# Kernel optimization log

Measured on AMD Instinct MI355X. Metric: run time of the kernel, lower is better.

## Reference

```python
import jax, jax.numpy as jnp
import numpy as np

BN_EPS = 1e-5

def _batchnorm(h, gamma, beta):
    # PyTorch BatchNorm1d in training mode: biased batch statistics over dim 0
    mu = jnp.mean(h, axis=0)
    var = jnp.mean((h - mu) ** 2, axis=0)
    return (h - mu) * jax.lax.rsqrt(var + BN_EPS) * gamma + beta


def setup_inputs() -> dict:
    key = jax.random.key(0)
    ks = jax.random.split(key, 8)
    N, E, D = 50000, 800000, 128
    x = jax.random.normal(ks[0], (N, D), dtype=jnp.float32)
    edge_index = jax.random.randint(ks[1], (2, E), 0, N, dtype=jnp.int64)
    s1 = 1.0 / np.sqrt(D)
    W1 = jax.random.uniform(ks[2], (D, D), jnp.float32, -s1, s1)
    b1 = jax.random.uniform(ks[3], (D,), jnp.float32, -s1, s1)
    W2 = jax.random.uniform(ks[4], (D, D), jnp.float32, -s1, s1)
    b2 = jax.random.uniform(ks[5], (D,), jnp.float32, -s1, s1)
    g1 = jnp.ones((D,), jnp.float32); beta1 = jnp.zeros((D,), jnp.float32)
    g2 = jnp.ones((D,), jnp.float32); beta2 = jnp.zeros((D,), jnp.float32)
    eps = jnp.array([0.1], jnp.float32)
    return {"x": x, "edge_index": edge_index, "eps": eps,
            "W1": W1, "b1": b1, "g1": g1, "beta1": beta1,
            "W2": W2, "b2": b2, "g2": g2, "beta2": beta2}


def reference(x, edge_index, eps, W1, b1, g1, beta1, W2, b2, g2, beta2):
    src, dst = edge_index[0], edge_index[1]
    N = x.shape[0]
    # gather by src, scatter-add to dst
    aggr = jax.ops.segment_sum(x[src], dst, num_segments=N)
    out = (1.0 + eps) * x + aggr  # eps broadcast (shape [1])
    h = jax.nn.relu(_batchnorm(out @ W1 + b1, g1, beta1))
    h = jax.nn.relu(_batchnorm(h @ W2 + b2, g2, beta2))
    return h
```

## Files before the change

kernel.cpp:

```cpp
#include <hip/hip_runtime.h>

#define D 128
#define FB2 8192
#define GCAP 512
#define NBMAX 3328
#define SCAN_PER 13

typedef __attribute__((ext_vector_type(8))) short short8;
typedef __attribute__((ext_vector_type(4))) float f32x4;

static __device__ __forceinline__ unsigned short f2bf(float f) {
    union { float f; unsigned u; } v; v.f = f;
    unsigned r = v.u + 0x7FFF + ((v.u >> 16) & 1);
    return (unsigned short)(r >> 16);
}

static __device__ __forceinline__ float2 bfpair2f(unsigned p) {
    union { unsigned u; float f; } a, b;
    a.u = (p & 0xFFFFu) << 16;
    b.u = p & 0xFFFF0000u;
    return make_float2(a.f, b.f);
}

static __device__ __forceinline__ void acc2(f32x4& A, uint2 p) {
    union { unsigned u; float f; } t;
    float f0, f1, f2, f3;
    t.u = p.x << 16;          f0 = t.f;
    t.u = p.x & 0xFFFF0000u;  f1 = t.f;
    t.u = p.y << 16;          f2 = t.f;
    t.u = p.y & 0xFFFF0000u;  f3 = t.f;
    A[0] += f0; A[1] += f1; A[2] += f2; A[3] += f3;
}

static __device__ __forceinline__ void emit_row(
    unsigned* h0, int d, unsigned lane8, float epsv, uint2 xv, f32x4 A)
{
    union { unsigned u; float f; } t;
    float x0, x1, x2, x3;
    t.u = xv.x << 16;          x0 = t.f;
    t.u = xv.x & 0xFFFF0000u;  x1 = t.f;
    t.u = xv.y << 16;          x2 = t.f;
    t.u = xv.y & 0xFFFF0000u;  x3 = t.f;
    float r0 = fmaf(epsv, x0, A[0]);
    float r1 = fmaf(epsv, x1, A[1]);
    float r2 = fmaf(epsv, x2, A[2]);
    float r3 = fmaf(epsv, x3, A[3]);
    uint2 o;
    o.x = (unsigned)f2bf(r0) | ((unsigned)f2bf(r1) << 16);
    o.y = (unsigned)f2bf(r2) | ((unsigned)f2bf(r3) << 16);
    *(uint2*)((char*)h0 + ((unsigned)(d * 256) + lane8)) = o;
}

__global__ __launch_bounds__(256) void prep_kernel(
    const float4* __restrict__ x4, uint2* __restrict__ xh, int xtotal,
    const float* __restrict__ W1, const float* __restrict__ W2,
    unsigned short* __restrict__ Wf1, unsigned short* __restrict__ Wf2,
    float* __restrict__ stats, int* __restrict__ bucketCount,
    unsigned short* __restrict__ zrow, int xblocks)
{
    if (blockIdx.x < (unsigned)xblocks) {
        int i = blockIdx.x * 256 + threadIdx.x;
        if (i >= xtotal) return;
        float4 v = x4[i];
        uint2 o;
        o.x = (unsigned)f2bf(v.x) | ((unsigned)f2bf(v.y) << 16);
        o.y = (unsigned)f2bf(v.z) | ((unsigned)f2bf(v.w) << 16);
        xh[i] = o;
    } else if (blockIdx.x < (unsigned)(xblocks + 128)) {
        int idx = (blockIdx.x - xblocks) * 256 + threadIdx.x;
        const float* W = (idx < 16384) ? W1 : W2;
        unsigned short* Wf = (idx < 16384) ? Wf1 : Wf2;
        int e = idx & 16383;
        int j = e & 7, lane = (e >> 3) & 63, ckk = e >> 9;
        int ct = ckk & 7, kk = ckk >> 3;
        int k = kk * 32 + (lane >> 4) * 8 + j;
        int n = ct * 16 + (lane & 15);
        Wf[e] = f2bf(W[k * 128 + n]);
    } else {
        int t = threadIdx.x;
        stats[t] = 0.f; stats[t + 256] = 0.f;
        for (int i = t; i < NBMAX; i += 256) bucketCount[i] = 0;
        if (t < 128) zrow[t] = 0;
    }
}

__global__ __launch_bounds__(256) void bucket_hist_kernel(
    const int* __restrict__ ei, int E, int NB2, int* __restrict__ bucketCount)
{
    __shared__ int hist[NBMAX];
    int tid = threadIdx.x;
    for (int i = tid; i < NB2; i += 256) hist[i] = 0;
    __syncthreads();
    int b0 = blockIdx.x * FB2;
    int lim = min(FB2, E - b0);
    for (int i = tid; i < lim; i += 256)
        atomicAdd(&hist[ei[E + b0 + i] >> 4], 1);
    __syncthreads();
    for (int i = tid; i < NB2; i += 256)
        if (hist[i]) atomicAdd(&bucketCount[i], hist[i]);
}

__global__ __launch_bounds__(256) void bucket_scan_kernel(
    const int* __restrict__ bucketCount, int NB2, int E,
    int* __restrict__ bucketBase, int* __restrict__ bucketCursor)
{
    __shared__ int part[256];
    int tid = threadIdx.x;
    int loc[SCAN_PER];
    int s = 0;
    #pragma unroll
    for (int j = 0; j < SCAN_PER; ++j) {
        int idx = tid * SCAN_PER + j;
        int v = (idx < NB2) ? bucketCount[idx] : 0;
        loc[j] = s;
        s += v;
    }
    part[tid] = s;
    __syncthreads();
    #pragma unroll
    for (int off = 1; off < 256; off <<= 1) {
        int u = (tid >= off) ? part[tid - off] : 0;
        __syncthreads();
        part[tid] += u;
        __syncthreads();
    }
    int tb = (tid > 0) ? part[tid - 1] : 0;
    #pragma unroll
    for (int j = 0; j < SCAN_PER; ++j) {
        int idx = tid * SCAN_PER + j;
        if (idx < NB2) {
            int ex = tb + loc[j];
            bucketBase[idx] = ex;
            bucketCursor[idx] = ex;
        }
    }
    if (tid == 0) bucketBase[NB2] = E;
}

__global__ __launch_bounds__(256) void bucket_fill_kernel(
    const int* __restrict__ ei, int E, int NB2,
    int* __restrict__ bucketCursor, unsigned* __restrict__ rec)
{
    __shared__ int hist[NBMAX], base[NBMAX];
    int tid = threadIdx.x;
    int b0 = blockIdx.x * FB2;
    for (int i = tid; i < NB2; i += 256) hist[i] = 0;
    __syncthreads();
    int lim = min(FB2, E - b0);
    for (int i = tid; i < lim; i += 256)
        atomicAdd(&hist[ei[E + b0 + i] >> 4], 1);
    __syncthreads();
    for (int i = tid; i < NB2; i += 256) {
        int c = hist[i];
        base[i] = c ? atomicAdd(&bucketCursor[i], c) : 0;
        hist[i] = 0;
    }
    __syncthreads();
    for (int i = tid; i < lim; i += 256) {
        int e = b0 + i;
        int dst = ei[E + e], src = ei[e];
        int bk = dst >> 4;
        int r = atomicAdd(&hist[bk], 1);
        rec[base[bk] + r] = ((unsigned)src << 4) | (unsigned)(dst & 15);
    }
}

__global__ __launch_bounds__(256) void bucket_gather_kernel(
    const unsigned* __restrict__ xh, const unsigned* __restrict__ rec,
    const int* __restrict__ bucketBase, const float* __restrict__ epsp,
    unsigned* __restrict__ h0, int N, int zoff)
{
    int g = blockIdx.x;
    int tid = threadIdx.x;
    int d0 = g << 4;

    __shared__ int cnts[16], rnk[16], offs[17];
    __shared__ int slist[GCAP + 8];

    if (tid < 16) { cnts[tid] = 0; rnk[tid] = 0; }
    for (int i = tid; i < GCAP + 8; i += 256) slist[i] = zoff;
    __syncthreads();

    int lo = bucketBase[g], hi = bucketBase[g + 1];
    for (int i = lo + tid; i < hi; i += 256)
        atomicAdd(&cnts[rec[i] & 15], 1);
    __syncthreads();
    if (tid == 0) {
        int run = 0;
        #pragma unroll
        for (int i = 0; i < 16; ++i) {
            offs[i] = run;
            run += (cnts[i] + 7) & ~7;
            if (run > GCAP) run = GCAP;
        }
        offs[16] = run;
    }
    __syncthreads();
    for (int i = lo + tid; i < hi; i += 256) {
        unsigned r = rec[i];
        int d = r & 15;
        int rk = atomicAdd(&rnk[d], 1);
        int pos = offs[d] + rk;
        if (pos < offs[d + 1]) slist[pos] = (int)((r >> 4) << 8);
    }
    __syncthreads();

    int wv = tid >> 6, lane = tid & 63;
    int half = lane >> 5, l5 = lane & 31;
    unsigned lane8 = (unsigned)(l5 << 3);
    float epsv = 1.0f + __ldg(epsp);
    const char* xc = (const char*)xh;

    int dloc = wv * 4;
    int dA = d0 + dloc, dB = dA + 1, dC = dA + 2, dD = dA + 3;
    int vA = (dA < N), vB = (dB < N), vC = (dC < N), vD = (dD < N);

    int s0 = offs[dloc + 0], s1 = offs[dloc + 1];
    int s2 = offs[dloc + 2], s3 = offs[dloc + 3], s4 = offs[dloc + 4];
    int nch0 = (s1 - s0) >> 3, nch1 = (s2 - s1) >> 3;
    int nch2 = (s3 - s2) >> 3, nch3 = (s4 - s3) >> 3;
    int iters = max(max(nch0, nch1), max(nch2, nch3));

    uint2 xv0 = *(const uint2*)(xc + (unsigned)((vA ? dA : 0) * 256) + lane8);
    uint2 xv1 = *(const uint2*)(xc + (unsigned)((vB ? dB : 0) * 256) + lane8);
    uint2 xv2 = *(const uint2*)(xc + (unsigned)((vC ? dC : 0) * 256) + lane8);
    uint2 xv3 = *(const uint2*)(xc + (unsigned)((vD ? dD : 0) * 256) + lane8);

    f32x4 A0 = (f32x4){0.f, 0.f, 0.f, 0.f};
    f32x4 A1 = (f32x4){0.f, 0.f, 0.f, 0.f};
    f32x4 A2 = (f32x4){0.f, 0.f, 0.f, 0.f};
    f32x4 A3 = (f32x4){0.f, 0.f, 0.f, 0.f};

    for (int c = 0; c < iters; ++c) {
        int b0 = (c < nch0) ? (s0 + (c << 3)) : GCAP;
        int b1 = (c < nch1) ? (s1 + (c << 3)) : GCAP;
        int b2 = (c < nch2) ? (s2 + (c << 3)) : GCAP;
        int b3 = (c < nch3) ? (s3 + (c << 3)) : GCAP;
        uint2 p0[4], p1[4], p2[4], p3[4];
        #pragma unroll
        for (int k = 0; k < 4; ++k) {
            unsigned o0 = (unsigned)slist[b0 + 2 * k + half];
            unsigned o1 = (unsigned)slist[b1 + 2 * k + half];
            unsigned o2 = (unsigned)slist[b2 + 2 * k + half];
            unsigned o3 = (unsigned)slist[b3 + 2 * k + half];
            p0[k] = *(const uint2*)(xc + (o0 + lane8));
            p1[k] = *(const uint2*)(xc + (o1 + lane8));
            p2[k] = *(const uint2*)(xc + (o2 + lane8));
            p3[k] = *(const uint2*)(xc + (o3 + lane8));
        }
        #pragma unroll
        for (int k = 0; k < 4; ++k) {
            acc2(A0, p0[k]); acc2(A1, p1[k]);
            acc2(A2, p2[k]); acc2(A3, p3[k]);
        }
    }

    #pragma unroll
    for (int r = 0; r < 4; ++r) {
        A0[r] += __shfl_xor(A0[r], 32, 64);
        A1[r] += __shfl_xor(A1[r], 32, 64);
        A2[r] += __shfl_xor(A2[r], 32, 64);
        A3[r] += __shfl_xor(A3[r], 32, 64);
    }

    if (half == 0) {
        if (vA) emit_row(h0, dA, lane8, epsv, xv0, A0);
        if (vB) emit_row(h0, dB, lane8, epsv, xv1, A1);
        if (vC) emit_row(h0, dC, lane8, epsv, xv2, A2);
        if (vD) emit_row(h0, dD, lane8, epsv, xv3, A3);
    }
}

static __device__ __forceinline__ short8 bn_relu_pack(
    const unsigned short* arow, int c, const float* scf, const float* shf)
{
    uint4 rw = *(const uint4*)(arow + c);
    float2 p0 = bfpair2f(rw.x), p1 = bfpair2f(rw.y);
    float2 p2 = bfpair2f(rw.z), p3 = bfpair2f(rw.w);
    p0.x = fmaxf(fmaf(p0.x, scf[c + 0], shf[c + 0]), 0.f);
    p0.y = fmaxf(fmaf(p0.y, scf[c + 1], shf[c + 1]), 0.f);
    p1.x = fmaxf(fmaf(p1.x, scf[c + 2], shf[c + 2]), 0.f);
    p1.y = fmaxf(fmaf(p1.y, scf[c + 3], shf[c + 3]), 0.f);
    p2.x = fmaxf(fmaf(p2.x, scf[c + 4], shf[c + 4]), 0.f);
    p2.y = fmaxf(fmaf(p2.y, scf[c + 5], shf[c + 5]), 0.f);
    p3.x = fmaxf(fmaf(p3.x, scf[c + 6], shf[c + 6]), 0.f);
    p3.y = fmaxf(fmaf(p3.y, scf[c + 7], shf[c + 7]), 0.f);
    short8 af;
    af[0] = (short)f2bf(p0.x); af[1] = (short)f2bf(p0.y);
    af[2] = (short)f2bf(p1.x); af[3] = (short)f2bf(p1.y);
    af[4] = (short)f2bf(p2.x); af[5] = (short)f2bf(p2.y);
    af[6] = (short)f2bf(p3.x); af[7] = (short)f2bf(p3.y);
    return af;
}

__global__ __launch_bounds__(256) void gemm_bn_mfma_kernel(
    const unsigned short* __restrict__ a_bf,
    const float* __restrict__ stat_in, const float* __restrict__ gamma,
    const float* __restrict__ beta, float invN,
    const unsigned short* __restrict__ Wf, const float* __restrict__ bias,
    unsigned short* __restrict__ zout,
    float* __restrict__ stat_sum, float* __restrict__ stat_sq,
    int N, int mode)
{
    __shared__ unsigned short Wl[16384];
    __shared__ float part[1024];
    __shared__ float scf[128], shf[128];

    int tid = threadIdx.x;
    {
        float4* dst = (float4*)Wl;
        const float4* srcp = (const float4*)Wf;
        #pragma unroll
        for (int i = 0; i < 8; ++i) dst[tid + i * 256] = srcp[tid + i * 256];
    }
    if (mode == 1 && tid < 128) {
        float mean = stat_in[tid] * invN;
        float var  = stat_in[128 + tid] * invN - mean * mean;
        float sv = gamma[tid] * rsqrtf(var + 1e-5f);
        scf[tid] = sv;
        shf[tid] = fmaf(-mean, sv, beta[tid]);
    }
    __syncthreads();

    int w = tid >> 6, lane = tid & 63, q = lane >> 4, n16 = lane & 15;
    int rowb = blockIdx.x * 128 + w * 16;
    int m0 = rowb + n16;
    int m1 = rowb + 64 + n16;
    int mc0 = (m0 < N) ? m0 : (N - 1);
    int mc1 = (m1 < N) ? m1 : (N - 1);
    const unsigned short* arow0 = a_bf + (size_t)mc0 * D;
    const unsigned short* arow1 = a_bf + (size_t)mc1 * D;

    f32x4 acc0[8], acc1[8];
    #pragma unroll
    for (int ct = 0; ct < 8; ++ct) {
        acc0[ct] = (f32x4){0.f, 0.f, 0.f, 0.f};
        acc1[ct] = (f32x4){0.f, 0.f, 0.f, 0.f};
    }

    #pragma unroll
    for (int kk = 0; kk < 4; ++kk) {
        int c = kk * 32 + q * 8;
        short8 af0, af1;
        if (mode == 0) {
            af0 = *(const short8*)(arow0 + c);
            af1 = *(const short8*)(arow1 + c);
        } else {
            af0 = bn_relu_pack(arow0, c, scf, shf);
            af1 = bn_relu_pack(arow1, c, scf, shf);
        }
        #pragma unroll
        for (int ct = 0; ct < 8; ++ct) {
            short8 bf = *(const short8*)&Wl[(((kk * 8 + ct) * 64) + lane) * 8];
            acc0[ct] = __builtin_amdgcn_mfma_f32_16x16x32_bf16(af0, bf, acc0[ct], 0, 0, 0);
            acc1[ct] = __builtin_amdgcn_mfma_f32_16x16x32_bf16(af1, bf, acc1[ct], 0, 0, 0);
        }
    }

    #pragma unroll
    for (int ct = 0; ct < 8; ++ct) {
        int col = ct * 16 + n16;
        float bv = __ldg(bias + col);
        float s = 0.f, qs = 0.f;
        #pragma unroll
        for (int reg = 0; reg < 4; ++reg) {
            int row = rowb + q * 4 + reg;
            float v = acc0[ct][reg] + bv;
            if (row < N) {
                zout[(size_t)row * D + col] = f2bf(v);
                s += v;
                qs = fmaf(v, v, qs);
            }
        }
        #pragma unroll
        for (int reg = 0; reg < 4; ++reg) {
            int row = rowb + 64 + q * 4 + reg;
            float v = acc1[ct][reg] + bv;
            if (row < N) {
                zout[(size_t)row * D + col] = f2bf(v);
                s += v;
                qs = fmaf(v, v, qs);
            }
        }
        s  += __shfl_xor(s, 16, 64);
        s  += __shfl_xor(s, 32, 64);
        qs += __shfl_xor(qs, 16, 64);
        qs += __shfl_xor(qs, 32, 64);
        if (lane < 16) {
            part[w * 128 + col] = s;
            part[512 + w * 128 + col] = qs;
        }
    }
    __syncthreads();

    if (tid < 128) {
        float s  = part[tid] + part[128 + tid] + part[256 + tid] + part[384 + tid];
        float qq = part[512 + tid] + part[640 + tid] + part[768 + tid] + part[896 + tid];
        atomicAdd(&stat_sum[tid], s);
        atomicAdd(&stat_sq[tid], qq);
    }
}

__global__ __launch_bounds__(256) void bn_relu_kernel(
    const uint2* __restrict__ z2, float4* __restrict__ out,
    const float* __restrict__ stat2, const float* __restrict__ gamma,
    const float* __restrict__ beta, float invN, int total4)
{
    __shared__ float sf[128], tf[128];
    int tid = threadIdx.x;
    if (tid < 128) {
        float mean = stat2[tid] * invN;
        float var  = stat2[128 + tid] * invN - mean * mean;
        float sv = gamma[tid] * rsqrtf(var + 1e-5f);
        sf[tid] = sv;
        tf[tid] = fmaf(-mean, sv, beta[tid]);
    }
    __syncthreads();

    int i = blockIdx.x * 256 + tid;
    if (i >= total4) return;
    uint2 zp = z2[i];
    float2 v01 = bfpair2f(zp.x);
    float2 v23 = bfpair2f(zp.y);
    int c = (i & 31) * 4;
    float4 o;
    o.x = fmaxf(fmaf(v01.x, sf[c + 0], tf[c + 0]), 0.f);
    o.y = fmaxf(fmaf(v01.y, sf[c + 1], tf[c + 1]), 0.f);
    o.z = fmaxf(fmaf(v23.x, sf[c + 2], tf[c + 2]), 0.f);
    o.w = fmaxf(fmaf(v23.y, sf[c + 3], tf[c + 3]), 0.f);
    out[i] = o;
}

extern "C" void kernel_launch(void* const* d_in, const int* in_sizes, int n_in,
                              void* d_out, int out_size, void* d_ws, size_t ws_size,
                              hipStream_t stream)
{
    const float* x   = (const float*)d_in[0];
    const int*   ei  = (const int*)d_in[1];
    const float* eps = (const float*)d_in[2];
    const float* W1  = (const float*)d_in[3];
    const float* b1  = (const float*)d_in[4];
    const float* g1  = (const float*)d_in[5];
    const float* be1 = (const float*)d_in[6];
    const float* W2  = (const float*)d_in[7];
    const float* b2  = (const float*)d_in[8];
    const float* g2  = (const float*)d_in[9];
    const float* be2 = (const float*)d_in[10];

    int N = in_sizes[0] / D;
    int E = in_sizes[1] / 2;
    size_t ND = (size_t)N * D;
    int NB2 = (N + 15) >> 4;

    unsigned short* xh  = (unsigned short*)d_ws;
    unsigned short* z1  = xh;
    unsigned short* region2 = xh + ND + 128;
    unsigned* rec       = (unsigned*)region2;
    unsigned short* z2  = region2;
    int* bucketCount    = (int*)((char*)region2 + (4 << 20));
    int* bucketBase     = bucketCount + NBMAX;
    int* bucketCursor   = bucketBase + NBMAX + 1;
    float* stats        = (float*)(region2 + ND);
    unsigned short* Wf1 = (unsigned short*)(stats + 512);
    unsigned short* Wf2 = Wf1 + 16384;

    float* sum1 = stats + 0,   *sq1 = stats + 128;
    float* sum2 = stats + 256, *sq2 = stats + 384;
    unsigned short* h0 = (unsigned short*)d_out;

    int xtotal = N * 32;
    int xblocks = (xtotal + 255) / 256;
    prep_kernel<<<xblocks + 129, 256, 0, stream>>>(
        (const float4*)x, (uint2*)xh, xtotal, W1, W2, Wf1, Wf2,
        stats, bucketCount, xh + ND, xblocks);

    int fblocks = (E + FB2 - 1) / FB2;
    bucket_hist_kernel<<<fblocks, 256, 0, stream>>>(ei, E, NB2, bucketCount);
    bucket_scan_kernel<<<1, 256, 0, stream>>>(bucketCount, NB2, E, bucketBase, bucketCursor);
    bucket_fill_kernel<<<fblocks, 256, 0, stream>>>(ei, E, NB2, bucketCursor, rec);
    bucket_gather_kernel<<<NB2, 256, 0, stream>>>(
        (const unsigned*)xh, rec, bucketBase, eps, (unsigned*)h0, N, N * 256);

    int gblocks = (N + 127) / 128;
    gemm_bn_mfma_kernel<<<gblocks, 256, 0, stream>>>(
        h0, nullptr, nullptr, nullptr, 0.f,
        Wf1, b1, z1, sum1, sq1, N, 0);
    gemm_bn_mfma_kernel<<<gblocks, 256, 0, stream>>>(
        z1, sum1, g1, be1, 1.0f / N,
        Wf2, b2, z2, sum2, sq2, N, 1);
    bn_relu_kernel<<<(N * 32 + 255) / 256, 256, 0, stream>>>(
        (const uint2*)z2, (float4*)d_out, sum2, g2, be2, 1.0f / N, N * 32);
}
```

Measured before the change: 229.5 us.

## Switch to two-level bucket sort with coarse buckets and replicated BN stat accumulators

Edges are now bucketed into 128-destination coarse buckets (about 391 instead of about 3125), which shrinks the shared histograms and the scan. A new subsort pass then orders each bucket by destination and records per-destination offsets, so the gather kernel no longer recounts or ranks edges with shared atomics. BN statistic accumulation is also spread across 4 replicated slots chosen by block index to cut global atomic contention, and readers sum the replicas. The cost is an extra kernel launch plus an extra pass over the edge records through a second buffer. There is also an aliasing risk: rec2 sits at an 8 MB offset inside region2, so it may overlap the bucket arrays or z2 for large E.

```diff
diff --git a/kernel.cpp b/kernel.cpp
--- a/kernel.cpp
+++ b/kernel.cpp
@@ -3,8 +3,7 @@
 #define D 128
 #define FB2 8192
 #define GCAP 512
-#define NBMAX 3328
-#define SCAN_PER 13
+#define NREP 4
 
 typedef __attribute__((ext_vector_type(8))) short short8;
 typedef __attribute__((ext_vector_type(4))) float f32x4;
@@ -78,79 +77,67 @@
         Wf[e] = f2bf(W[k * 128 + n]);
     } else {
         int t = threadIdx.x;
-        stats[t] = 0.f; stats[t + 256] = 0.f;
-        for (int i = t; i < NBMAX; i += 256) bucketCount[i] = 0;
+        #pragma unroll
+        for (int i = 0; i < 2 * NREP; ++i) stats[t + i * 256] = 0.f;
+        bucketCount[t] = 0; bucketCount[t + 256] = 0;
         if (t < 128) zrow[t] = 0;
     }
 }
 
 __global__ __launch_bounds__(256) void bucket_hist_kernel(
-    const int* __restrict__ ei, int E, int NB2, int* __restrict__ bucketCount)
-{
-    __shared__ int hist[NBMAX];
+    const int* __restrict__ ei, int E, int NB, int* __restrict__ bucketCount)
+{
+    __shared__ int hist[512];
     int tid = threadIdx.x;
-    for (int i = tid; i < NB2; i += 256) hist[i] = 0;
+    for (int i = tid; i < NB; i += 256) hist[i] = 0;
     __syncthreads();
     int b0 = blockIdx.x * FB2;
     int lim = min(FB2, E - b0);
     for (int i = tid; i < lim; i += 256)
-        atomicAdd(&hist[ei[E + b0 + i] >> 4], 1);
-    __syncthreads();
-    for (int i = tid; i < NB2; i += 256)
+        atomicAdd(&hist[ei[E + b0 + i] >> 7], 1);
+    __syncthreads();
+    for (int i = tid; i < NB; i += 256)
         if (hist[i]) atomicAdd(&bucketCount[i], hist[i]);
 }
 
-__global__ __launch_bounds__(256) void bucket_scan_kernel(
-    const int* __restrict__ bucketCount, int NB2, int E,
+__global__ __launch_bounds__(512) void bucket_scan_kernel(
+    const int* __restrict__ bucketCount, int NB, int E,
     int* __restrict__ bucketBase, int* __restrict__ bucketCursor)
 {
-    __shared__ int part[256];
+    __shared__ int sm[512];
     int tid = threadIdx.x;
-    int loc[SCAN_PER];
-    int s = 0;
+    int v = (tid < NB) ? bucketCount[tid] : 0;
+    sm[tid] = v;
+    __syncthreads();
     #pragma unroll
-    for (int j = 0; j < SCAN_PER; ++j) {
-        int idx = tid * SCAN_PER + j;
-        int v = (idx < NB2) ? bucketCount[idx] : 0;
-        loc[j] = s;
-        s += v;
-    }
-    part[tid] = s;
-    __syncthreads();
-    #pragma unroll
-    for (int off = 1; off < 256; off <<= 1) {
-        int u = (tid >= off) ? part[tid - off] : 0;
+    for (int off = 1; off < 512; off <<= 1) {
+        int u = (tid >= off) ? sm[tid - off] : 0;
         __syncthreads();
-        part[tid] += u;
+        sm[tid] += u;
         __syncthreads();
     }
-    int tb = (tid > 0) ? part[tid - 1] : 0;
-    #pragma unroll
-    for (int j = 0; j < SCAN_PER; ++j) {
-        int idx = tid * SCAN_PER + j;
-        if (idx < NB2) {
-            int ex = tb + loc[j];
-            bucketBase[idx] = ex;
-            bucketCursor[idx] = ex;
-        }
-    }
-    if (tid == 0) bucketBase[NB2] = E;
+    if (tid < NB) {
+        int ex = sm[tid] - v;
+        bucketBase[tid] = ex;
+        bucketCursor[tid] = ex;
+    }
+    if (tid == 0) bucketBase[NB] = E;
 }
 
 __global__ __launch_bounds__(256) void bucket_fill_kernel(
-    const int* __restrict__ ei, int E, int NB2,
+    const int* __restrict__ ei, int E, int NB,
     int* __restrict__ bucketCursor, unsigned* __restrict__ rec)
 {
-    __shared__ int hist[NBMAX], base[NBMAX];
+    __shared__ int hist[512], base[512];
     int tid = threadIdx.x;
     int b0 = blockIdx.x * FB2;
-    for (int i = tid; i < NB2; i += 256) hist[i] = 0;
+    for (int i = tid; i < NB; i += 256) hist[i] = 0;
     __syncthreads();
     int lim = min(FB2, E - b0);
     for (int i = tid; i < lim; i += 256)
-        atomicAdd(&hist[ei[E + b0 + i] >> 4], 1);
-    __syncthreads();
-    for (int i = tid; i < NB2; i += 256) {
+        atomicAdd(&hist[ei[E + b0 + i] >> 7], 1);
+    __syncthreads();
+    for (int i = tid; i < NB; i += 256) {
         int c = hist[i];
         base[i] = c ? atomicAdd(&bucketCursor[i], c) : 0;
         hist[i] = 0;
@@ -159,49 +146,70 @@
     for (int i = tid; i < lim; i += 256) {
         int e = b0 + i;
         int dst = ei[E + e], src = ei[e];
-        int bk = dst >> 4;
+        int bk = dst >> 7;
         int r = atomicAdd(&hist[bk], 1);
-        rec[base[bk] + r] = ((unsigned)src << 4) | (unsigned)(dst & 15);
+        rec[base[bk] + r] = ((unsigned)src << 7) | (unsigned)(dst & 127);
+    }
+}
+
+__global__ __launch_bounds__(256) void subsort_kernel(
+    const unsigned* __restrict__ rec, const int* __restrict__ bucketBase,
+    unsigned* __restrict__ rec2, int* __restrict__ dstOff)
+{
+    __shared__ int cnt[128], pref[128], rnk[128];
+    int b = blockIdx.x, tid = threadIdx.x;
+    int lo = bucketBase[b], hi = bucketBase[b + 1];
+    if (tid < 128) { cnt[tid] = 0; rnk[tid] = 0; }
+    __syncthreads();
+    for (int i = lo + tid; i < hi; i += 256)
+        atomicAdd(&cnt[rec[i] & 127], 1);
+    __syncthreads();
+    if (tid == 0) {
+        int run = 0;
+        #pragma unroll
+        for (int j = 0; j < 128; ++j) { pref[j] = run; run += cnt[j]; }
+    }
+    __syncthreads();
+    if (tid < 128) dstOff[b * 128 + tid] = lo + pref[tid];
+    for (int i = lo + tid; i < hi; i += 256) {
+        unsigned r = rec[i];
+        int d = r & 127;
+        int rk = atomicAdd(&rnk[d], 1);
+        rec2[lo + pref[d] + rk] = ((r >> 7) << 8) | (unsigned)(d & 15);
     }
 }
 
 __global__ __launch_bounds__(256) void bucket_gather_kernel(
-    const unsigned* __restrict__ xh, const unsigned* __restrict__ rec,
-    const int* __restrict__ bucketBase, const float* __restrict__ epsp,
+    const unsigned* __restrict__ xh, const unsigned* __restrict__ rec2,
+    const int* __restrict__ dstOff, const float* __restrict__ epsp,
     unsigned* __restrict__ h0, int N, int zoff)
 {
     int g = blockIdx.x;
     int tid = threadIdx.x;
     int d0 = g << 4;
 
-    __shared__ int cnts[16], rnk[16], offs[17];
+    __shared__ int doff[17], offs[17];
     __shared__ int slist[GCAP + 8];
 
-    if (tid < 16) { cnts[tid] = 0; rnk[tid] = 0; }
+    if (tid < 17) doff[tid] = dstOff[d0 + tid];
     for (int i = tid; i < GCAP + 8; i += 256) slist[i] = zoff;
-    __syncthreads();
-
-    int lo = bucketBase[g], hi = bucketBase[g + 1];
-    for (int i = lo + tid; i < hi; i += 256)
-        atomicAdd(&cnts[rec[i] & 15], 1);
     __syncthreads();
     if (tid == 0) {
         int run = 0;
         #pragma unroll
-        for (int i = 0; i < 16; ++i) {
-            offs[i] = run;
-            run += (cnts[i] + 7) & ~7;
+        for (int j = 0; j < 16; ++j) {
+            offs[j] = run;
+            run += (doff[j + 1] - doff[j] + 7) & ~7;
             if (run > GCAP) run = GCAP;
         }
         offs[16] = run;
     }
     __syncthreads();
-    for (int i = lo + tid; i < hi; i += 256) {
-        unsigned r = rec[i];
-        int d = r & 15;
-        int rk = atomicAdd(&rnk[d], 1);
-        int pos = offs[d] + rk;
-        if (pos < offs[d + 1]) slist[pos] = (int)((r >> 4) << 8);
+    for (int i = doff[0] + tid; i < doff[16]; i += 256) {
+        unsigned r = rec2[i];
+        int dl = r & 15;
+        int slot = offs[dl] + (i - doff[dl]);
+        if (slot < offs[dl + 1]) slist[slot] = (int)(r & 0xFFFFFF00u);
     }
     __syncthreads();
 
@@ -314,8 +322,14 @@
         for (int i = 0; i < 8; ++i) dst[tid + i * 256] = srcp[tid + i * 256];
     }
     if (mode == 1 && tid < 128) {
-        float mean = stat_in[tid] * invN;
-        float var  = stat_in[128 + tid] * invN - mean * mean;
+        float ssum = 0.f, sqs = 0.f;
+        #pragma unroll
+        for (int r = 0; r < NREP; ++r) {
+            ssum += stat_in[r * 512 + tid];
+            sqs  += stat_in[r * 512 + 128 + tid];
+        }
+        float mean = ssum * invN;
+        float var  = sqs * invN - mean * mean;
         float sv = gamma[tid] * rsqrtf(var + 1e-5f);
         scf[tid] = sv;
         shf[tid] = fmaf(-mean, sv, beta[tid]);
@@ -394,10 +408,11 @@
     __syncthreads();
 
     if (tid < 128) {
+        int rep = ((int)blockIdx.x & (NREP - 1)) * 512;
         float s  = part[tid] + part[128 + tid] + part[256 + tid] + part[384 + tid];
         float qq = part[512 + tid] + part[640 + tid] + part[768 + tid] + part[896 + tid];
-        atomicAdd(&stat_sum[tid], s);
-        atomicAdd(&stat_sq[tid], qq);
+        atomicAdd(&stat_sum[rep + tid], s);
+        atomicAdd(&stat_sq[rep + tid], qq);
     }
 }
 
@@ -409,8 +424,14 @@
     __shared__ float sf[128], tf[128];
     int tid = threadIdx.x;
     if (tid < 128) {
-        float mean = stat2[tid] * invN;
-        float var  = stat2[128 + tid] * invN - mean * mean;
+        float ssum = 0.f, sqs = 0.f;
+        #pragma unroll
+        for (int r = 0; r < NREP; ++r) {
+            ssum += stat2[r * 512 + tid];
+            sqs  += stat2[r * 512 + 128 + tid];
+        }
+        float mean = ssum * invN;
+        float var  = sqs * invN - mean * mean;
         float sv = gamma[tid] * rsqrtf(var + 1e-5f);
         sf[tid] = sv;
         tf[tid] = fmaf(-mean, sv, beta[tid]);
@@ -450,7 +471,8 @@
     int N = in_sizes[0] / D;
     int E = in_sizes[1] / 2;
     size_t ND = (size_t)N * D;
-    int NB2 = (N + 15) >> 4;
+    int NB  = (N + 127) >> 7;
+    int NG  = (N + 15) >> 4;
 
     unsigned short* xh  = (unsigned short*)d_ws;
     unsigned short* z1  = xh;
@@ -458,10 +480,12 @@
     unsigned* rec       = (unsigned*)region2;
     unsigned short* z2  = region2;
     int* bucketCount    = (int*)((char*)region2 + (4 << 20));
-    int* bucketBase     = bucketCount + NBMAX;
-    int* bucketCursor   = bucketBase + NBMAX + 1;
+    int* bucketBase     = bucketCount + 512;
+    int* bucketCursor   = bucketBase + 513;
+    int* dstOff         = bucketCursor + 512;
+    unsigned* rec2      = (unsigned*)((char*)region2 + (8 << 20));
     float* stats        = (float*)(region2 + ND);
-    unsigned short* Wf1 = (unsigned short*)(stats + 512);
+    unsigned short* Wf1 = (unsigned short*)(stats + 2 * NREP * 256);
     unsigned short* Wf2 = Wf1 + 16384;
 
     float* sum1 = stats + 0,   *sq1 = stats + 128;
@@ -475,11 +499,12 @@
         stats, bucketCount, xh + ND, xblocks);
 
     int fblocks = (E + FB2 - 1) / FB2;
-    bucket_hist_kernel<<<fblocks, 256, 0, stream>>>(ei, E, NB2, bucketCount);
-    bucket_scan_kernel<<<1, 256, 0, stream>>>(bucketCount, NB2, E, bucketBase, bucketCursor);
-    bucket_fill_kernel<<<fblocks, 256, 0, stream>>>(ei, E, NB2, bucketCursor, rec);
-    bucket_gather_kernel<<<NB2, 256, 0, stream>>>(
-        (const unsigned*)xh, rec, bucketBase, eps, (unsigned*)h0, N, N * 256);
+    bucket_hist_kernel<<<fblocks, 256, 0, stream>>>(ei, E, NB, bucketCount);
+    bucket_scan_kernel<<<1, 512, 0, stream>>>(bucketCount, NB, E, bucketBase, bucketCursor);
+    bucket_fill_kernel<<<fblocks, 256, 0, stream>>>(ei, E, NB, bucketCursor, rec);
+    subsort_kernel<<<NB, 256, 0, stream>>>(rec, bucketBase, rec2, dstOff);
+    bucket_gather_kernel<<<NG, 256, 0, stream>>>(
+        (const unsigned*)xh, rec2, dstOff, eps, (unsigned*)h0, N, N * 256);
 
     int gblocks = (N + 127) / 128;
     gemm_bn_mfma_kernel<<<gblocks, 256, 0, stream>>>(
```

Measured after the change: 215.0 us. 1.07x faster.
